# Performance work log

Hardware: AMD Instinct MI355X
Metric: run time of the kernel (lower is better)

The kernel has to match this reference:

```python
import jax, jax.numpy as jnp
import numpy as np

GRID_SIZE = 5   # efficient-kan default
K = 3           # spline_order
BATCH = 32768
OBS_DIM = 128
ACTION_DIM = 18
# (in_features, out_features) for the 7 KANLinear layers:
# base: 128->256->256->64 ; adv head: 64->64->18 ; value head: 64->64->1
DIMS = [(OBS_DIM, 256), (256, 256), (256, 64), (64, 64), (64, ACTION_DIM), (64, 64), (64, 1)]


def make_grid(in_f):
    # uniform grid on [-1,1] extended by K knots each side: shape (in_f, GRID_SIZE+2K+1)
    h = 2.0 / GRID_SIZE
    g = jnp.arange(-K, GRID_SIZE + K + 1, dtype=jnp.float32) * h - 1.0
    return jnp.broadcast_to(g, (in_f, g.shape[0]))


def b_splines(x, grid):
    # Cox-de Boor recursion; x: (B, in) -> bases (B, in, GRID_SIZE+K)
    xe = x[:, :, None]
    b = ((xe >= grid[:, :-1]) & (xe < grid[:, 1:])).astype(x.dtype)
    for j in range(1, K + 1):
        left = (xe - grid[:, : -(j + 1)]) / (grid[:, j:-1] - grid[:, : -(j + 1)])
        right = (grid[:, j + 1:] - xe) / (grid[:, j + 1:] - grid[:, 1:-j])
        b = left * b[:, :, :-1] + right * b[:, :, 1:]
    return b


def kan_layer(x, bw, sw, sc):
    # efficient-kan KANLinear: silu base path + spline path with standalone scaler
    grid = make_grid(x.shape[1])
    base = jax.nn.silu(x) @ bw.T                              # (B, out)
    bases = b_splines(x, grid)                                # (B, in, G+K)
    spline = jnp.einsum('big,oig->bo', bases, sw * sc[:, :, None])
    return base + spline


def setup_inputs() -> dict:
    key = jax.random.key(0)
    ks = jax.random.split(key, 1 + 3 * len(DIMS))
    inp = {"x": jax.random.normal(ks[0], (BATCH, OBS_DIM), dtype=jnp.float32)}
    for i, (fin, fout) in enumerate(DIMS):
        inp[f"bw{i}"] = jax.random.normal(ks[1 + 3 * i], (fout, fin), dtype=jnp.float32) / np.sqrt(fin).astype(np.float32)
        inp[f"sw{i}"] = jax.random.normal(ks[2 + 3 * i], (fout, fin, GRID_SIZE + K), dtype=jnp.float32) * (0.1 / np.sqrt(fin).astype(np.float32))
        inp[f"sc{i}"] = 1.0 + 0.1 * jax.random.normal(ks[3 + 3 * i], (fout, fin), dtype=jnp.float32)
    return inp


def reference(x, bw0, sw0, sc0, bw1, sw1, sc1, bw2, sw2, sc2,
              bw3, sw3, sc3, bw4, sw4, sc4, bw5, sw5, sc5, bw6, sw6, sc6):
    h = x
    for bw, sw, sc in [(bw0, sw0, sc0), (bw1, sw1, sc1), (bw2, sw2, sc2)]:
        h = kan_layer(h, bw, sw, sc)
    advantage = kan_layer(kan_layer(h, bw3, sw3, sc3), bw4, sw4, sc4)
    state_value = kan_layer(kan_layer(h, bw5, sw5, sc5), bw6, sw6, sc6)
    return (advantage, state_value)
```

## Files before the change

kernel.cpp:

```cpp
#include <hip/hip_runtime.h>

typedef unsigned short u16;
typedef unsigned int   u32;
typedef unsigned long long u64;
typedef __bf16 bf16;
typedef float f32x4  __attribute__((ext_vector_type(4)));
typedef bf16  bf16x8 __attribute__((ext_vector_type(8)));

__device__ __forceinline__ float bf2f(u16 u){ return (float)__builtin_bit_cast(bf16,u); }
__device__ __forceinline__ u16   f2bf(float f){ return __builtin_bit_cast(u16,(bf16)f); }
__device__ __forceinline__ u32   pkbf(float a,float b){ return (u32)f2bf(a)|((u32)f2bf(b)<<16); }

#define NROWS 32768

__device__ __forceinline__ uint4 basis_pk(float x)
{
  float tp  = __fmaf_rn(x, 2.5f, 5.5f);
  float tpc = fminf(fmaxf(tp, -1.0f), 12.0f);
  float fi  = floorf(tpc);
  float uu  = tpc - fi;
  int   i0  = (int)fi;
  float u2 = uu*uu, u3 = u2*uu, w1 = 1.0f-uu, w2 = w1*w1, w3 = w2*w1;
  float d1 = __fmaf_rn(3.0f, u3, __fmaf_rn(-6.0f, u2, 4.0f));
  float d2 = __fmaf_rn(3.0f, w3, __fmaf_rn(-6.0f, w2, 4.0f));
  u64 dpk = (u64)pkbf(w3, d1) | ((u64)pkbf(d2, u3) << 32);
  int ss = i0*16 - 48;
  u64 A  = dpk << (ss & 63);
  u64 Bv = dpk >> ((64-ss) & 63);
  u64 Cv = dpk << ((ss-64) & 63);
  u64 Dv = dpk >> ((-ss) & 63);
  u64 lo = (ss>=0 && ss<64)   ? A  : ((ss<0 && ss>-64) ? Dv : 0ull);
  u64 hi = (ss>=64 && ss<128) ? Cv : ((ss>0 && ss<64)  ? Bv : 0ull);
  uint4 r; r.x=(u32)lo; r.y=(u32)(lo>>32); r.z=(u32)hi; r.w=(u32)(hi>>32);
  return r;
}

__device__ __forceinline__ void expand9(float x, u16& sil, uint4& bpk)
{
  float s = x * (1.0f/(1.0f+__expf(-x)));
  sil = f2bf(s);
  bpk = basis_pk(x);
}
__device__ __forceinline__ void expand10(float x, u32& spk, uint4& bpk)
{
  float s = x * (1.0f/(1.0f+__expf(-x)));
  u16 uh = f2bf(s);
  u16 ul = f2bf(s - bf2f(uh));
  spk = (u32)uh | ((u32)ul<<16);
  bpk = basis_pk(x);
}

struct PrepArgs {
  const float* bw[7]; const float* sw[7]; const float* sc[7];
  u16* w[7];
  int cin[7]; int coutr[7]; int ntsh[7]; int fmt[7];
  u32 elems[7];
};

__global__ __launch_bounds__(256) void prep_kernel(PrepArgs pa)
{
  u32 idx = blockIdx.x*256 + threadIdx.x;
  int L = 0;
  u32 off = idx;
  while (L < 6 && off >= pa.elems[L]) { off -= pa.elems[L]; ++L; }
  int j    = off & 7;
  int lane = (off>>3) & 63;
  u32 tl   = off >> 9;
  int ntsh = pa.ntsh[L];
  u32 kstep = tl >> ntsh;
  int ntile = (int)(tl & ((1u<<ntsh)-1u));
  int o    = ntile*16 + (lane&15);
  int kpos = (lane>>4)*8 + j;
  int i = 0, g = 0; bool sil;
  if (pa.fmt[L] == 0){
    u32 c = kstep/9u; int r = (int)(kstep - c*9u);
    if (r == 0){ i = (int)c*32 + kpos; sil = true; }
    else { int kl=(r-1)*32+kpos; i=(int)c*32+(kl>>3); g=kl&7; sil = false; }
  } else {
    u32 c = kstep/5u; int r = (int)(kstep - c*5u);
    if (r == 0){ i = (int)c*16 + (kpos>>1); sil = true; }
    else { int kl=(r-1)*32+kpos; i=(int)c*16+(kl>>3); g=kl&7; sil = false; }
  }
  float v = 0.f;
  if (o < pa.coutr[L]) {
    size_t e = (size_t)o*pa.cin[L] + i;
    v = sil ? pa.bw[L][e] : pa.sw[L][e*8+g]*pa.sc[L][e]*0.16666666666666666f;
  }
  pa.w[L][off] = f2bf(v);
}

template<int CIN,int COUT,int IN_MODE,int OUT_MODE>
__global__ __launch_bounds__(512,4) void kan_layer(const void* __restrict__ hin_,
    const u16* __restrict__ W, void* __restrict__ hout_)
{
  constexpr int NCH = CIN/32;
  constexpr int TOTK = NCH*9;
  constexpr int NTILES = COUT/16;
  constexpr int NT = (COUT>=128)? COUT/128 : 1;
  constexpr int SROW=20, BROW=132, BOFF=64*SROW;
  constexpr int CHUNK = BOFF + 64*BROW;
  __shared__ u32 buf[2][CHUNK];

  const int b0 = blockIdx.x*64;
  const int tid = threadIdx.x;
  const int wave = tid>>6, lane = tid&63, m = lane&15, quad = lane>>4;

  const u16*   __restrict__ hb = (const u16*)hin_;
  const float* __restrict__ hf = (const float*)hin_;

  f32x4 acc[4][NT];
#pragma unroll
  for (int a=0;a<4;++a)
#pragma unroll
    for (int n=0;n<NT;++n) acc[a][n]=(f32x4){0.f,0.f,0.f,0.f};

  bf16x8 bbuf[3][NT];
  auto loadB = [&](int kstep, bf16x8* dst){
    if (kstep < TOTK){
#pragma unroll
      for (int nt=0; nt<NT; ++nt)
        dst[nt] = *(const bf16x8*)(W + (((size_t)kstep*NTILES + ((wave*NT+nt)&(NTILES-1)))*64 + lane)*8);
    }
  };
  loadB(0, bbuf[0]); loadB(1, bbuf[1]);

  float xb[2][4];
  auto loadX = [&](int kc, float* dst){
#pragma unroll
    for (int t=0;t<4;++t){
      int task = t*512+tid, row = task>>5, f = task&31;
      int gi = (b0+row)*CIN + kc*32 + f;
      dst[t] = (IN_MODE==0)? hf[gi] : bf2f(hb[gi]);
    }
  };
  auto expandChunk = [&](const float* xc, u32* dstb){
#pragma unroll
    for (int t=0;t<4;++t){
      int task=t*512+tid, row=task>>5, f=task&31;
      u16 sil; uint4 bpk;
      expand9(xc[t], sil, bpk);
      ((u16*)dstb)[row*(SROW*2) + f] = sil;
      *(uint4*)&dstb[BOFF + row*BROW + f*4] = bpk;
    }
  };

  loadX(0, xb[0]);
  expandChunk(xb[0], buf[0]);
  if (NCH > 1) loadX(1, xb[1]);
  __syncthreads();

  for (int kc=0; kc<NCH; ++kc){
    u32* cur = buf[kc&1];
    u32* nxt = buf[(kc+1)&1];
    if (kc+1 < NCH) expandChunk(xb[(kc+1)&1], nxt);
    if (kc+2 < NCH) loadX(kc+2, xb[kc&1]);
#pragma unroll
    for (int ks=0; ks<9; ++ks){
      const int kstep = kc*9 + ks;
      loadB(kstep+2, bbuf[2]);
      bf16x8 af[4];
#pragma unroll
      for (int mt=0; mt<4; ++mt){
        int row = mt*16 + m;
        af[mt] = (ks==0)
          ? *(const bf16x8*)&cur[row*SROW + quad*4]
          : *(const bf16x8*)&cur[BOFF + row*BROW + (ks-1)*16 + quad*4];
      }
#pragma unroll
      for (int nt=0; nt<NT; ++nt)
#pragma unroll
        for (int mt=0; mt<4; ++mt)
          acc[mt][nt] = __builtin_amdgcn_mfma_f32_16x16x32_bf16(af[mt], bbuf[0][nt], acc[mt][nt],0,0,0);
#pragma unroll
      for (int nt=0; nt<NT; ++nt){ bbuf[0][nt]=bbuf[1][nt]; bbuf[1][nt]=bbuf[2][nt]; }
    }
    __syncthreads();
  }

  if (wave*NT < NTILES){
#pragma unroll
    for (int mt=0; mt<4; ++mt)
#pragma unroll
      for (int nt=0; nt<NT; ++nt)
#pragma unroll
        for (int r=0; r<4; ++r){
          size_t off = (size_t)(b0 + mt*16 + quad*4 + r)*COUT + ((wave*NT+nt)&(NTILES-1))*16 + m;
          if constexpr (OUT_MODE==0) ((float*)hout_)[off] = acc[mt][nt][r];
          else                       ((u16*)hout_)[off]   = f2bf(acc[mt][nt][r]);
        }
  }
}

template<int IN_MODE>
__global__ __launch_bounds__(512,4) void tail_kernel(const void* __restrict__ h2_,
  const u16* __restrict__ W3, const u16* __restrict__ W4,
  const u16* __restrict__ W5, const u16* __restrict__ W6,
  float* __restrict__ out_adv, float* __restrict__ out_val)
{
  constexpr int SROW=20, BROW=68, BOFF=64*20;
  __shared__ u32   Aexp[BOFF + 64*BROW];
  __shared__ float hA[64*65], hV[64*65];

  const int b0 = blockIdx.x*64;
  const int tid = threadIdx.x;
  const int wave = tid>>6, lane = tid&63, m = lane&15, quad = lane>>4;
  const int rg = wave>>2, cg = wave&3;

  const u16*   __restrict__ hb = (const u16*)h2_;
  const float* __restrict__ hf = (const float*)h2_;

  f32x4 a3[2], a5[2];
#pragma unroll
  for (int mt=0;mt<2;++mt){ a3[mt]=(f32x4){0,0,0,0}; a5[mt]=(f32x4){0,0,0,0}; }

  bf16x8 w3b[3], w5b[3];
  auto loadB2 = [&](int kstep, int d){
    if (kstep < 20){
      size_t bi = (((size_t)kstep*4 + cg)*64 + lane)*8;
      w3b[d] = *(const bf16x8*)(W3+bi);
      w5b[d] = *(const bf16x8*)(W5+bi);
    }
  };
  loadB2(0,0); loadB2(1,1);

  float xb[2][2];
  auto loadX = [&](int kc, float* dst){
#pragma unroll
    for (int t=0;t<2;++t){
      int task = t*512+tid, row=task>>4, f=task&15;
      int gi = (b0+row)*64 + kc*16 + f;
      dst[t] = (IN_MODE==0)? hf[gi] : bf2f(hb[gi]);
    }
  };
  loadX(0, xb[0]);

  for (int kc=0; kc<4; ++kc){
    const float* xc = xb[kc&1];
#pragma unroll
    for (int t=0;t<2;++t){
      int task=t*512+tid, row=task>>4, f=task&15;
      u32 spk; uint4 bpk;
      expand10(xc[t], spk, bpk);
      Aexp[row*SROW + f] = spk;
      *(uint4*)&Aexp[BOFF + row*BROW + f*4] = bpk;
    }
    if (kc+1 < 4) loadX(kc+1, xb[(kc+1)&1]);
    __syncthreads();
#pragma unroll
    for (int ks=0; ks<5; ++ks){
      const int kstep = kc*5 + ks;
      loadB2(kstep+2, 2);
      bf16x8 af[2];
#pragma unroll
      for (int mt=0; mt<2; ++mt){
        int row = rg*32 + mt*16 + m;
        af[mt] = (ks==0)
          ? *(const bf16x8*)&Aexp[row*SROW + quad*4]
          : *(const bf16x8*)&Aexp[BOFF + row*BROW + (ks-1)*16 + quad*4];
      }
#pragma unroll
      for (int mt=0; mt<2; ++mt){
        a3[mt] = __builtin_amdgcn_mfma_f32_16x16x32_bf16(af[mt], w3b[0], a3[mt],0,0,0);
        a5[mt] = __builtin_amdgcn_mfma_f32_16x16x32_bf16(af[mt], w5b[0], a5[mt],0,0,0);
      }
      w3b[0]=w3b[1]; w3b[1]=w3b[2]; w5b[0]=w5b[1]; w5b[1]=w5b[2];
    }
    __syncthreads();
  }
#pragma unroll
  for (int mt=0;mt<2;++mt)
#pragma unroll
    for (int r=0;r<4;++r){
      int row = rg*32 + mt*16 + quad*4 + r;
      hA[row*65 + cg*16 + m] = a3[mt][r];
      hV[row*65 + cg*16 + m] = a5[mt][r];
    }
  __syncthreads();

  f32x4 a4[2];
#pragma unroll
  for (int mt=0;mt<2;++mt) a4[mt]=(f32x4){0,0,0,0};
  bf16x8 w4b[3];
  auto loadB4 = [&](int kstep, int d){
    if (kstep < 20) w4b[d] = *(const bf16x8*)(W4 + (((size_t)kstep*4 + cg)*64 + lane)*8);
  };
  loadB4(0,0); loadB4(1,1);
  for (int kc=0; kc<4; ++kc){
#pragma unroll
    for (int t=0;t<2;++t){
      int task=t*512+tid, row=task>>4, f=task&15;
      u32 spk; uint4 bpk;
      expand10(hA[row*65 + kc*16 + f], spk, bpk);
      Aexp[row*SROW + f] = spk;
      *(uint4*)&Aexp[BOFF + row*BROW + f*4] = bpk;
    }
    __syncthreads();
#pragma unroll
    for (int ks=0; ks<5; ++ks){
      loadB4(kc*5+ks+2, 2);
      bf16x8 af[2];
#pragma unroll
      for (int mt=0; mt<2; ++mt){
        int row = rg*32 + mt*16 + m;
        af[mt] = (ks==0)
          ? *(const bf16x8*)&Aexp[row*SROW + quad*4]
          : *(const bf16x8*)&Aexp[BOFF + row*BROW + (ks-1)*16 + quad*4];
      }
#pragma unroll
      for (int mt=0; mt<2; ++mt)
        a4[mt] = __builtin_amdgcn_mfma_f32_16x16x32_bf16(af[mt], w4b[0], a4[mt],0,0,0);
      w4b[0]=w4b[1]; w4b[1]=w4b[2];
    }
    __syncthreads();
  }
  {
    int col = cg*16 + m;
    if (col < 18){
#pragma unroll
      for (int mt=0;mt<2;++mt)
#pragma unroll
        for (int r=0;r<4;++r)
          out_adv[(size_t)(b0 + rg*32 + mt*16 + quad*4 + r)*18 + col] = a4[mt][r];
    }
  }

  f32x4 a6[2];
#pragma unroll
  for (int mt=0;mt<2;++mt) a6[mt]=(f32x4){0,0,0,0};
  bf16x8 w6b[3];
  auto loadB6 = [&](int kstep, int d){
    if (kstep < 20) w6b[d] = *(const bf16x8*)(W6 + (((size_t)kstep*4 + cg)*64 + lane)*8);
  };
  loadB6(0,0); loadB6(1,1);
  for (int kc=0; kc<4; ++kc){
#pragma unroll
    for (int t=0;t<2;++t){
      int task=t*512+tid, row=task>>4, f=task&15;
      u32 spk; uint4 bpk;
      expand10(hV[row*65 + kc*16 + f], spk, bpk);
      Aexp[row*SROW + f] = spk;
      *(uint4*)&Aexp[BOFF + row*BROW + f*4] = bpk;
    }
    __syncthreads();
#pragma unroll
    for (int ks=0; ks<5; ++ks){
      loadB6(kc*5+ks+2, 2);
      bf16x8 af[2];
#pragma unroll
      for (int mt=0; mt<2; ++mt){
        int row = rg*32 + mt*16 + m;
        af[mt] = (ks==0)
          ? *(const bf16x8*)&Aexp[row*SROW + quad*4]
          : *(const bf16x8*)&Aexp[BOFF + row*BROW + (ks-1)*16 + quad*4];
      }
#pragma unroll
      for (int mt=0; mt<2; ++mt)
        a6[mt] = __builtin_amdgcn_mfma_f32_16x16x32_bf16(af[mt], w6b[0], a6[mt],0,0,0);
      w6b[0]=w6b[1]; w6b[1]=w6b[2];
    }
    __syncthreads();
  }
  if (cg==0 && m==0){
#pragma unroll
    for (int mt=0;mt<2;++mt)
#pragma unroll
      for (int r=0;r<4;++r)
        out_val[b0 + rg*32 + mt*16 + quad*4 + r] = a6[mt][r];
  }
}

extern "C" void kernel_launch(void* const* d_in, const int* in_sizes, int n_in,
                              void* d_out, int out_size, void* d_ws, size_t ws_size,
                              hipStream_t stream)
{
  (void)in_sizes; (void)n_in; (void)out_size;
  char* ws = (char*)d_ws;

  const size_t wbytes[7] = {589824u, 1179648u, 294912u, 81920u, 81920u, 81920u, 81920u};
  const bool midf32 = ws_size >= 77889536u;

  u16* W[7];
  char *h0, *h1, *h2;
  if (midf32) {
    h0 = ws;
    h1 = h0 + 33554432u;
    h2 = h1 + 33554432u;
    size_t off = 75497472u;
    for (int l=0;l<7;++l){ W[l] = (u16*)(ws+off); off += wbytes[l]; }
  } else {
    h0 = ws;
    h1 = h0 + 16777216u;
    h2 = h1 + 16777216u;
    size_t off = 37748736u;
    for (int l=0;l<7;++l){ W[l] = (u16*)(ws+off); off += wbytes[l]; }
  }

  PrepArgs pa;
  const int cins[7]   = {128,256,256,64,64,64,64};
  const int coutr[7]  = {256,256,64,64,18,64,1};
  const int ntsh[7]   = {4,4,2,2,2,2,2};
  const int fmts[7]   = {0,0,0,1,1,1,1};
  const u32 elems[7]  = {294912u,589824u,147456u,40960u,40960u,40960u,40960u};
  for (int l=0;l<7;++l){
    pa.bw[l] = (const float*)d_in[1+3*l];
    pa.sw[l] = (const float*)d_in[2+3*l];
    pa.sc[l] = (const float*)d_in[3+3*l];
    pa.w[l]  = W[l];
    pa.cin[l]=cins[l]; pa.coutr[l]=coutr[l]; pa.ntsh[l]=ntsh[l]; pa.fmt[l]=fmts[l];
    pa.elems[l]=elems[l];
  }
  prep_kernel<<<4672, 256, 0, stream>>>(pa);

  dim3 g(NROWS/64), b(512);
  float* out_adv = (float*)d_out;
  float* out_val = (float*)d_out + (size_t)NROWS*18;
  if (midf32) {
    kan_layer<128,256,0,0><<<g,b,0,stream>>>(d_in[0], W[0], h0);
    kan_layer<256,256,0,0><<<g,b,0,stream>>>(h0, W[1], h1);
    kan_layer<256, 64,0,0><<<g,b,0,stream>>>(h1, W[2], h2);
    tail_kernel<0><<<g,b,0,stream>>>(h2, W[3], W[4], W[5], W[6], out_adv, out_val);
  } else {
    kan_layer<128,256,0,1><<<g,b,0,stream>>>(d_in[0], W[0], h0);
    kan_layer<256,256,1,1><<<g,b,0,stream>>>(h0, W[1], h1);
    kan_layer<256, 64,1,1><<<g,b,0,stream>>>(h1, W[2], h2);
    tail_kernel<1><<<g,b,0,stream>>>(h2, W[3], W[4], W[5], W[6], out_adv, out_val);
  }
}
```

Before: 227.2 us.

## Use 4-wave blocks with a configurable wave grid and prefetch A fragments

Each layer block now runs 256 threads (4 waves) instead of 512, and the waves are arranged in a GR x GC grid that tiles both rows and output columns. This removes the idle waves the old layout had for COUT=64 and gives each wave more N tiles, so each A fragment read from LDS is reused across more MFMAs. A fragments for the next k-step are loaded from LDS one step early to hide LDS latency. In exchange each thread expands twice as many inputs, registers per thread go up, and fewer waves per block may reduce latency hiding.

```diff
diff --git a/kernel.cpp b/kernel.cpp
--- a/kernel.cpp
+++ b/kernel.cpp
@@ -89,14 +89,15 @@
   pa.w[L][off] = f2bf(v);
 }
 
-template<int CIN,int COUT,int IN_MODE,int OUT_MODE>
-__global__ __launch_bounds__(512,4) void kan_layer(const void* __restrict__ hin_,
+template<int CIN,int COUT,int GR,int GC,int IN_MODE,int OUT_MODE>
+__global__ __launch_bounds__(256,2) void kan_layer(const void* __restrict__ hin_,
     const u16* __restrict__ W, void* __restrict__ hout_)
 {
   constexpr int NCH = CIN/32;
   constexpr int TOTK = NCH*9;
   constexpr int NTILES = COUT/16;
-  constexpr int NT = (COUT>=128)? COUT/128 : 1;
+  constexpr int MT  = 4/GR;
+  constexpr int NTL = NTILES/GC;
   constexpr int SROW=20, BROW=132, BOFF=64*SROW;
   constexpr int CHUNK = BOFF + 64*BROW;
   __shared__ u32 buf[2][CHUNK];
@@ -104,43 +105,54 @@
   const int b0 = blockIdx.x*64;
   const int tid = threadIdx.x;
   const int wave = tid>>6, lane = tid&63, m = lane&15, quad = lane>>4;
+  const int rg = wave / GC, cg = wave % GC;
+  const int rbase = rg*(MT*16);
 
   const u16*   __restrict__ hb = (const u16*)hin_;
   const float* __restrict__ hf = (const float*)hin_;
 
-  f32x4 acc[4][NT];
-#pragma unroll
-  for (int a=0;a<4;++a)
-#pragma unroll
-    for (int n=0;n<NT;++n) acc[a][n]=(f32x4){0.f,0.f,0.f,0.f};
-
-  bf16x8 bbuf[3][NT];
+  f32x4 acc[MT][NTL];
+#pragma unroll
+  for (int a=0;a<MT;++a)
+#pragma unroll
+    for (int n=0;n<NTL;++n) acc[a][n]=(f32x4){0.f,0.f,0.f,0.f};
+
+  bf16x8 bbuf[3][NTL];
   auto loadB = [&](int kstep, bf16x8* dst){
     if (kstep < TOTK){
 #pragma unroll
-      for (int nt=0; nt<NT; ++nt)
-        dst[nt] = *(const bf16x8*)(W + (((size_t)kstep*NTILES + ((wave*NT+nt)&(NTILES-1)))*64 + lane)*8);
+      for (int nt=0; nt<NTL; ++nt)
+        dst[nt] = *(const bf16x8*)(W + (((size_t)kstep*NTILES + (cg*NTL+nt))*64 + lane)*8);
     }
   };
   loadB(0, bbuf[0]); loadB(1, bbuf[1]);
 
-  float xb[2][4];
+  float xb[2][8];
   auto loadX = [&](int kc, float* dst){
 #pragma unroll
-    for (int t=0;t<4;++t){
-      int task = t*512+tid, row = task>>5, f = task&31;
+    for (int t=0;t<8;++t){
+      int task = t*256+tid, row = task>>5, f = task&31;
       int gi = (b0+row)*CIN + kc*32 + f;
       dst[t] = (IN_MODE==0)? hf[gi] : bf2f(hb[gi]);
     }
   };
   auto expandChunk = [&](const float* xc, u32* dstb){
 #pragma unroll
-    for (int t=0;t<4;++t){
-      int task=t*512+tid, row=task>>5, f=task&31;
+    for (int t=0;t<8;++t){
+      int task=t*256+tid, row=task>>5, f=task&31;
       u16 sil; uint4 bpk;
       expand9(xc[t], sil, bpk);
       ((u16*)dstb)[row*(SROW*2) + f] = sil;
       *(uint4*)&dstb[BOFF + row*BROW + f*4] = bpk;
+    }
+  };
+  auto loadA = [&](const u32* cur, int ks, bf16x8* dst){
+#pragma unroll
+    for (int mt=0; mt<MT; ++mt){
+      int row = rbase + mt*16 + m;
+      dst[mt] = (ks==0)
+        ? *(const bf16x8*)&cur[row*SROW + quad*4]
+        : *(const bf16x8*)&cur[BOFF + row*BROW + (ks-1)*16 + quad*4];
     }
   };
 
@@ -154,41 +166,38 @@
     u32* nxt = buf[(kc+1)&1];
     if (kc+1 < NCH) expandChunk(xb[(kc+1)&1], nxt);
     if (kc+2 < NCH) loadX(kc+2, xb[kc&1]);
+    bf16x8 afc[MT], afn[MT];
+    loadA(cur, 0, afc);
 #pragma unroll
     for (int ks=0; ks<9; ++ks){
       const int kstep = kc*9 + ks;
       loadB(kstep+2, bbuf[2]);
-      bf16x8 af[4];
-#pragma unroll
-      for (int mt=0; mt<4; ++mt){
-        int row = mt*16 + m;
-        af[mt] = (ks==0)
-          ? *(const bf16x8*)&cur[row*SROW + quad*4]
-          : *(const bf16x8*)&cur[BOFF + row*BROW + (ks-1)*16 + quad*4];
-      }
-#pragma unroll
-      for (int nt=0; nt<NT; ++nt)
-#pragma unroll
-        for (int mt=0; mt<4; ++mt)
-          acc[mt][nt] = __builtin_amdgcn_mfma_f32_16x16x32_bf16(af[mt], bbuf[0][nt], acc[mt][nt],0,0,0);
-#pragma unroll
-      for (int nt=0; nt<NT; ++nt){ bbuf[0][nt]=bbuf[1][nt]; bbuf[1][nt]=bbuf[2][nt]; }
-    }
-    __syncthreads();
-  }
-
-  if (wave*NT < NTILES){
-#pragma unroll
-    for (int mt=0; mt<4; ++mt)
-#pragma unroll
-      for (int nt=0; nt<NT; ++nt)
-#pragma unroll
-        for (int r=0; r<4; ++r){
-          size_t off = (size_t)(b0 + mt*16 + quad*4 + r)*COUT + ((wave*NT+nt)&(NTILES-1))*16 + m;
-          if constexpr (OUT_MODE==0) ((float*)hout_)[off] = acc[mt][nt][r];
-          else                       ((u16*)hout_)[off]   = f2bf(acc[mt][nt][r]);
-        }
-  }
+      if (ks+1 < 9) loadA(cur, ks+1, afn);
+#pragma unroll
+      for (int nt=0; nt<NTL; ++nt)
+#pragma unroll
+        for (int mt=0; mt<MT; ++mt)
+          acc[mt][nt] = __builtin_amdgcn_mfma_f32_16x16x32_bf16(afc[mt], bbuf[0][nt], acc[mt][nt],0,0,0);
+#pragma unroll
+      for (int nt=0; nt<NTL; ++nt){ bbuf[0][nt]=bbuf[1][nt]; bbuf[1][nt]=bbuf[2][nt]; }
+      if (ks+1 < 9){
+#pragma unroll
+        for (int mt=0; mt<MT; ++mt) afc[mt]=afn[mt];
+      }
+    }
+    __syncthreads();
+  }
+
+#pragma unroll
+  for (int mt=0; mt<MT; ++mt)
+#pragma unroll
+    for (int nt=0; nt<NTL; ++nt)
+#pragma unroll
+      for (int r=0; r<4; ++r){
+        size_t off = (size_t)(b0 + rbase + mt*16 + quad*4 + r)*COUT + (cg*NTL+nt)*16 + m;
+        if constexpr (OUT_MODE==0) ((float*)hout_)[off] = acc[mt][nt][r];
+        else                       ((u16*)hout_)[off]   = f2bf(acc[mt][nt][r]);
+      }
 }
 
 template<int IN_MODE>
@@ -411,18 +420,18 @@
   }
   prep_kernel<<<4672, 256, 0, stream>>>(pa);
 
-  dim3 g(NROWS/64), b(512);
+  dim3 g(NROWS/64), bl(256), bt(512);
   float* out_adv = (float*)d_out;
   float* out_val = (float*)d_out + (size_t)NROWS*18;
   if (midf32) {
-    kan_layer<128,256,0,0><<<g,b,0,stream>>>(d_in[0], W[0], h0);
-    kan_layer<256,256,0,0><<<g,b,0,stream>>>(h0, W[1], h1);
-    kan_layer<256, 64,0,0><<<g,b,0,stream>>>(h1, W[2], h2);
-    tail_kernel<0><<<g,b,0,stream>>>(h2, W[3], W[4], W[5], W[6], out_adv, out_val);
+    kan_layer<128,256,1,4,0,0><<<g,bl,0,stream>>>(d_in[0], W[0], h0);
+    kan_layer<256,256,1,4,0,0><<<g,bl,0,stream>>>(h0, W[1], h1);
+    kan_layer<256, 64,2,2,0,0><<<g,bl,0,stream>>>(h1, W[2], h2);
+    tail_kernel<0><<<g,bt,0,stream>>>(h2, W[3], W[4], W[5], W[6], out_adv, out_val);
   } else {
-    kan_layer<128,256,0,1><<<g,b,0,stream>>>(d_in[0], W[0], h0);
-    kan_layer<256,256,1,1><<<g,b,0,stream>>>(h0, W[1], h1);
-    kan_layer<256, 64,1,1><<<g,b,0,stream>>>(h1, W[2], h2);
-    tail_kernel<1><<<g,b,0,stream>>>(h2, W[3], W[4], W[5], W[6], out_adv, out_val);
-  }
-}
+    kan_layer<128,256,1,4,0,1><<<g,bl,0,stream>>>(d_in[0], W[0], h0);
+    kan_layer<256,256,1,4,1,1><<<g,bl,0,stream>>>(h0, W[1], h1);
+    kan_layer<256, 64,2,2,1,1><<<g,bl,0,stream>>>(h1, W[2], h2);
+    tail_kernel<1><<<g,bt,0,stream>>>(h2, W[3], W[4], W[5], W[6], out_adv, out_val);
+  }
+}
```

Measured after the change: 263.2 us. 1.16x slower.
